# Optimization experiments

Hardware: AMD Instinct MI355X
Metric: run time of the kernel (lower is better)

The kernel has to match this reference:

```python
import jax, jax.numpy as jnp
import numpy as np

KNOTS = 16
BN_EPS = 1e-5  # flax BatchNorm default


def _normalize_spline_params(W, H, D):
    # widths/heights sum to 1 over the [0,1] hypercube; slopes positive
    dx = jax.nn.softmax(W, axis=-1)          # (N, d, K) bin widths
    dy = jax.nn.softmax(H, axis=-1)          # (N, d, K) bin heights
    sl = jax.nn.softplus(D)                  # (N, d, K-1) interior knot slopes
    return dx, dy, sl


def _gather_bin(a, idx):
    # a: (N, d, K'), idx: (N, d) -> (N, d)
    return jnp.take_along_axis(a, idx[..., None], axis=-1)[..., 0]


def _rqs_forward(t, dx, dy, sl):
    """Rational-quadratic spline on [0,1] (Durkan et al. 2019); identity outside.
    t: (N, d); dx, dy: (N, d, K); sl: (N, d, K-1).
    Returns y: (N, d), log_det: (N,)."""
    K = dx.shape[-1]
    zero = jnp.zeros_like(dx[..., :1])
    one = jnp.ones_like(dx[..., :1])
    xk = jnp.concatenate([zero, jnp.cumsum(dx, axis=-1)], axis=-1)   # (N, d, K+1) knot x
    yk = jnp.concatenate([zero, jnp.cumsum(dy, axis=-1)], axis=-1)   # (N, d, K+1) knot y
    dk = jnp.concatenate([one, sl, one], axis=-1)                    # (N, d, K+1) knot slopes

    in_bounds = (t >= 0.0) & (t <= 1.0)
    tc = jnp.clip(t, 0.0, 1.0)
    # per-element bin search (vectorized searchsorted)
    idx = jnp.clip(jnp.sum((tc[..., None] >= xk).astype(jnp.int32), axis=-1) - 1, 0, K - 1)

    xk_b = _gather_bin(xk, idx)
    yk_b = _gather_bin(yk, idx)
    dx_b = _gather_bin(dx, idx)
    dy_b = _gather_bin(dy, idx)
    d0 = _gather_bin(dk, idx)
    d1 = _gather_bin(dk, idx + 1)

    xi = (tc - xk_b) / dx_b            # position within bin, in [0,1]
    s = dy_b / dx_b                    # bin mean slope
    xi1m = xi * (1.0 - xi)
    den = s + (d0 + d1 - 2.0 * s) * xi1m
    y_in = yk_b + dy_b * (s * xi * xi + d0 * xi1m) / den
    dydx = s * s * (d1 * xi * xi + 2.0 * s * xi1m + d0 * (1.0 - xi) ** 2) / (den * den)

    y = jnp.where(in_bounds, y_in, t)
    log_det = jnp.sum(jnp.where(in_bounds, jnp.log(dydx), 0.0), axis=1)  # (N,)
    return y, log_det


def setup_inputs() -> dict:
    key = jax.random.key(0)
    ks = jax.random.split(key, 8)
    N, D, C = 65536, 64, 16
    d = D // 2
    spline_dim = 3 * KNOTS - 1
    cin = d + C           # conditioner input width: hstack(xc, c)
    H1, H2 = 128, 128     # layers=(128,128)

    def dense(k, fi, fo):
        return (jax.random.normal(k, (fi, fo), jnp.float32) / np.float32(np.sqrt(fi)))

    return {
        "x": jax.random.uniform(ks[0], (N, D), jnp.float32),
        "c": jax.random.normal(ks[1], (N, C), jnp.float32),
        "bn_scale": jnp.ones((cin,), jnp.float32),
        "bn_bias": jnp.zeros((cin,), jnp.float32),
        "bn_mean": 0.1 * jax.random.normal(ks[2], (cin,), jnp.float32),
        "bn_var": jax.random.uniform(ks[3], (cin,), jnp.float32, minval=0.5, maxval=1.5),
        "W0": dense(ks[4], cin, H1), "b0": jnp.zeros((H1,), jnp.float32),
        "W1": dense(ks[5], H1, H2), "b1": jnp.zeros((H2,), jnp.float32),
        "W2": dense(ks[6], H2, d * spline_dim), "b2": jnp.zeros((d * spline_dim,), jnp.float32),
    }


def reference(x, c, bn_scale, bn_bias, bn_mean, bn_var, W0, b0, W1, b1, W2, b2):
    N, D = x.shape
    d = D // 2
    xt, xc = x[:, :d], x[:, d:]
    h = jnp.hstack((xc, c))
    # BatchNorm in eval mode (use_running_average=True)
    h = (h - bn_mean) * jax.lax.rsqrt(bn_var + BN_EPS) * bn_scale + bn_bias
    h = jax.nn.swish(h @ W0 + b0)
    h = jax.nn.swish(h @ W1 + b1)
    p = (h @ W2 + b2).reshape(N, d, 3 * KNOTS - 1)
    dx, dy, sl = _normalize_spline_params(
        p[..., :KNOTS], p[..., KNOTS:2 * KNOTS], p[..., 2 * KNOTS:])
    yt, log_det = _rqs_forward(xt, dx, dy, sl)
    y = jnp.hstack((yt, xc))
    return y, log_det
```

## Files before the change

### kernel.cpp

```cpp
#include <hip/hip_runtime.h>
#include <math.h>

#define BN_EPS 1e-5f
#define ROWS 64

typedef __attribute__((ext_vector_type(8))) short short8;
typedef __attribute__((ext_vector_type(4))) float float4v;

__device__ __forceinline__ unsigned short f2bf(float f) {
    union { float f; unsigned int u; } v; v.f = f;
    unsigned int r = v.u + 0x7FFF + ((v.u >> 16) & 1);
    return (unsigned short)(r >> 16);
}
__device__ __forceinline__ float softplus_f(float v) {
    float r = log1pf(__expf(-fabsf(v)));
    return v > 0.f ? v + r : r;
}
__device__ __forceinline__ float swish_f(float a) {
    return a / (1.f + __expf(-a));
}

__global__ void prep_weights(const float* __restrict__ W0, const float* __restrict__ W1,
                             const float* __restrict__ W2,
                             unsigned short* __restrict__ Wt0, unsigned short* __restrict__ Wt1,
                             unsigned short* __restrict__ Wt2) {
    int e = blockIdx.x * 256 + threadIdx.x;
    if (e < 128 * 64) {
        int n = e >> 6, k = e & 63;
        Wt0[e] = f2bf(k < 48 ? W0[k * 128 + n] : 0.f);
        return;
    }
    e -= 128 * 64;
    if (e < 128 * 128) {
        int n = e >> 7, k = e & 127;
        Wt1[e] = f2bf(W1[k * 128 + n]);
        return;
    }
    e -= 128 * 128;
    if (e < 1536 * 128) {
        int col = e >> 7, k = e & 127;
        int d = col / 48, j = col - d * 48;
        Wt2[e] = f2bf(j < 47 ? W2[k * 1504 + d * 47 + j] : 0.f);
    }
}

__launch_bounds__(256, 2)
__global__ void nsc_mfma(const float* __restrict__ x, const float* __restrict__ c,
                         const float* __restrict__ bn_scale, const float* __restrict__ bn_bias,
                         const float* __restrict__ bn_mean, const float* __restrict__ bn_var,
                         const unsigned short* __restrict__ Wt0, const float* __restrict__ b0,
                         const unsigned short* __restrict__ Wt1, const float* __restrict__ b1,
                         const unsigned short* __restrict__ Wt2, const float* __restrict__ b2,
                         float* __restrict__ out, int N) {
    __shared__ char smem[70656];
    unsigned short* h0 = (unsigned short*)smem;
    unsigned short* h2 = (unsigned short*)smem;
    float*          yt = (float*)smem;
    float*          ldp = (float*)(smem + 8448);
    unsigned short* h1 = (unsigned short*)(smem + 17408);

    const int tid  = threadIdx.x;
    const int lane = tid & 63;
    const int l    = lane & 15;
    const int q    = lane >> 4;
    const int wu   = __builtin_amdgcn_readfirstlane(tid >> 6);
    const int r0   = blockIdx.x * ROWS;
    float* pw = (float*)(smem + 17408) + wu * (64 * 52);

    for (int idx = tid; idx < 64 * 64; idx += 256) {
        int r = idx >> 6, j = idx & 63;
        float h = 0.f;
        if (j < 48) {
            int row = r0 + r;
            float v = (j < 32) ? x[(size_t)row * 64 + 32 + j] : c[(size_t)row * 16 + (j - 32)];
            h = (v - bn_mean[j]) * rsqrtf(bn_var[j] + BN_EPS) * bn_scale[j] + bn_bias[j];
        }
        h0[r * 72 + j] = f2bf(h);
    }
    for (int idx = tid; idx < 64 * 32; idx += 256) {
        int r = idx >> 5, j = idx & 31;
        out[(size_t)(r0 + r) * 64 + 32 + j] = x[(size_t)(r0 + r) * 64 + 32 + j];
    }
    float xtreg[8];
    {
        const float* xrow = x + (size_t)(r0 + lane) * 64 + wu * 8;
        *(float4v*)(xtreg)     = *(const float4v*)(xrow);
        *(float4v*)(xtreg + 4) = *(const float4v*)(xrow + 4);
    }
    __syncthreads();

    {
        float4v acc[2][4];
        float4v z = {0.f, 0.f, 0.f, 0.f};
        #pragma unroll
        for (int nt = 0; nt < 2; ++nt)
            #pragma unroll
            for (int mt = 0; mt < 4; ++mt) acc[nt][mt] = z;
        #pragma unroll
        for (int ks = 0; ks < 2; ++ks) {
            short8 a[4];
            #pragma unroll
            for (int mt = 0; mt < 4; ++mt)
                a[mt] = *(const short8*)(h0 + (mt * 16 + l) * 72 + ks * 32 + (q << 3));
            #pragma unroll
            for (int nt = 0; nt < 2; ++nt) {
                int n0 = (wu * 2 + nt) * 16;
                short8 b = *(const short8*)(Wt0 + (n0 + l) * 64 + ks * 32 + (q << 3));
                #pragma unroll
                for (int mt = 0; mt < 4; ++mt)
                    acc[nt][mt] = __builtin_amdgcn_mfma_f32_16x16x32_bf16(a[mt], b, acc[nt][mt], 0, 0, 0);
            }
        }
        #pragma unroll
        for (int nt = 0; nt < 2; ++nt) {
            int n0 = (wu * 2 + nt) * 16;
            float bb = b0[n0 + l];
            #pragma unroll
            for (int mt = 0; mt < 4; ++mt)
                #pragma unroll
                for (int r = 0; r < 4; ++r)
                    h1[(mt * 16 + q * 4 + r) * 136 + n0 + l] = f2bf(swish_f(acc[nt][mt][r] + bb));
        }
    }
    __syncthreads();

    {
        float4v acc[2][4];
        float4v z = {0.f, 0.f, 0.f, 0.f};
        #pragma unroll
        for (int nt = 0; nt < 2; ++nt)
            #pragma unroll
            for (int mt = 0; mt < 4; ++mt) acc[nt][mt] = z;
        #pragma unroll
        for (int ks = 0; ks < 4; ++ks) {
            short8 a[4];
            #pragma unroll
            for (int mt = 0; mt < 4; ++mt)
                a[mt] = *(const short8*)(h1 + (mt * 16 + l) * 136 + ks * 32 + (q << 3));
            #pragma unroll
            for (int nt = 0; nt < 2; ++nt) {
                int n0 = (wu * 2 + nt) * 16;
                short8 b = *(const short8*)(Wt1 + (n0 + l) * 128 + ks * 32 + (q << 3));
                #pragma unroll
                for (int mt = 0; mt < 4; ++mt)
                    acc[nt][mt] = __builtin_amdgcn_mfma_f32_16x16x32_bf16(a[mt], b, acc[nt][mt], 0, 0, 0);
            }
        }
        #pragma unroll
        for (int nt = 0; nt < 2; ++nt) {
            int n0 = (wu * 2 + nt) * 16;
            float bb = b1[n0 + l];
            #pragma unroll
            for (int mt = 0; mt < 4; ++mt)
                #pragma unroll
                for (int r = 0; r < 4; ++r)
                    h2[(mt * 16 + q * 4 + r) * 136 + n0 + l] = f2bf(swish_f(acc[nt][mt][r] + bb));
        }
    }
    __syncthreads();

    short8 af[4][4];
    #pragma unroll
    for (int mt = 0; mt < 4; ++mt)
        #pragma unroll
        for (int ks = 0; ks < 4; ++ks)
            af[mt][ks] = *(const short8*)(h2 + (mt * 16 + l) * 136 + ks * 32 + (q << 3));
    __syncthreads();

    float ld_local = 0.f;
    for (int pass = 0; pass < 8; ++pass) {
        const int d  = wu * 8 + pass;
        const int cb = d * 48;
        float4v acc[3][4];
        float4v z = {0.f, 0.f, 0.f, 0.f};
        #pragma unroll
        for (int nt = 0; nt < 3; ++nt)
            #pragma unroll
            for (int mt = 0; mt < 4; ++mt) acc[nt][mt] = z;
        #pragma unroll
        for (int ks = 0; ks < 4; ++ks) {
            #pragma unroll
            for (int nt = 0; nt < 3; ++nt) {
                short8 b = *(const short8*)(Wt2 + (size_t)(cb + nt * 16 + l) * 128 + ks * 32 + (q << 3));
                #pragma unroll
                for (int mt = 0; mt < 4; ++mt)
                    acc[nt][mt] = __builtin_amdgcn_mfma_f32_16x16x32_bf16(af[mt][ks], b, acc[nt][mt], 0, 0, 0);
            }
        }
        #pragma unroll
        for (int nt = 0; nt < 3; ++nt) {
            int j = nt * 16 + l;
            float bj = (j < 47) ? b2[d * 47 + j] : 0.f;
            #pragma unroll
            for (int mt = 0; mt < 4; ++mt)
                #pragma unroll
                for (int r = 0; r < 4; ++r)
                    pw[(mt * 16 + q * 4 + r) * 52 + j] = acc[nt][mt][r] + bj;
        }
        asm volatile("s_waitcnt lgkmcnt(0)" ::: "memory");
        float pr[48];
        #pragma unroll
        for (int j = 0; j < 12; ++j)
            *(float4v*)(pr + j * 4) = *(const float4v*)(pw + lane * 52 + j * 4);

        float mWv = pr[0], mHv = pr[16];
        #pragma unroll
        for (int i = 1; i < 16; ++i) { mWv = fmaxf(mWv, pr[i]); mHv = fmaxf(mHv, pr[16 + i]); }
        float sW = 0.f, sH = 0.f;
        #pragma unroll
        for (int i = 0; i < 16; ++i) { pr[i] = __expf(pr[i] - mWv); sW += pr[i]; }
        #pragma unroll
        for (int i = 0; i < 16; ++i) { pr[16 + i] = __expf(pr[16 + i] - mHv); sH += pr[16 + i]; }
        float invW = 1.f / sW, invH = 1.f / sH;

        float t  = xtreg[pass];
        bool inb = (t >= 0.f) && (t <= 1.f);
        float tc = fminf(fmaxf(t, 0.f), 1.f);

        float cum = 0.f, cumy = 0.f, xkb = 0.f, ykb = 0.f;
        float dxb = pr[0] * invW, dyb = pr[16] * invH;
        int idx = 0;
        #pragma unroll
        for (int i = 0; i < 16; ++i) {
            float dxi = pr[i] * invW, dyi = pr[16 + i] * invH;
            bool cnd = (tc >= cum);
            idx = cnd ? i : idx;
            xkb = cnd ? cum : xkb;
            ykb = cnd ? cumy : ykb;
            dxb = cnd ? dxi : dxb;
            dyb = cnd ? dyi : dyb;
            cum  += dxi;
            cumy += dyi;
        }
        float a0 = 0.f, a1 = 0.f;
        #pragma unroll
        for (int j = 0; j < 15; ++j) {
            a0 = (j == idx - 1) ? pr[32 + j] : a0;
            a1 = (j == idx)     ? pr[32 + j] : a1;
        }
        float d0 = (idx == 0)  ? 1.f : softplus_f(a0);
        float d1 = (idx == 15) ? 1.f : softplus_f(a1);

        float xi  = (tc - xkb) / dxb;
        float s   = dyb / dxb;
        float xim = 1.f - xi;
        float x1m = xi * xim;
        float den = s + (d0 + d1 - 2.f * s) * x1m;
        float y_in = ykb + dyb * (s * xi * xi + d0 * x1m) / den;
        float dydx = s * s * (d1 * xi * xi + 2.f * s * x1m + d0 * xim * xim) / (den * den);

        yt[lane * 33 + d] = inb ? y_in : t;
        ld_local += inb ? __logf(dydx) : 0.f;
    }
    ldp[wu * 64 + lane] = ld_local;
    __syncthreads();

    for (int idx = tid; idx < 64 * 32; idx += 256) {
        int r = idx >> 5, j = idx & 31;
        out[(size_t)(r0 + r) * 64 + j] = yt[r * 33 + j];
    }
    if (tid < 64) {
        out[(size_t)N * 64 + r0 + tid] =
            ldp[tid] + ldp[64 + tid] + ldp[128 + tid] + ldp[192 + tid];
    }
}

extern "C" void kernel_launch(void* const* d_in, const int* in_sizes, int n_in,
                              void* d_out, int out_size, void* d_ws, size_t ws_size,
                              hipStream_t stream) {
    const float* x        = (const float*)d_in[0];
    const float* c        = (const float*)d_in[1];
    const float* bn_scale = (const float*)d_in[2];
    const float* bn_bias  = (const float*)d_in[3];
    const float* bn_mean  = (const float*)d_in[4];
    const float* bn_var   = (const float*)d_in[5];
    const float* W0       = (const float*)d_in[6];
    const float* b0       = (const float*)d_in[7];
    const float* W1       = (const float*)d_in[8];
    const float* b1       = (const float*)d_in[9];
    const float* W2       = (const float*)d_in[10];
    const float* b2       = (const float*)d_in[11];
    float* out = (float*)d_out;

    unsigned short* Wt0 = (unsigned short*)d_ws;
    unsigned short* Wt1 = Wt0 + 128 * 64;
    unsigned short* Wt2 = Wt1 + 128 * 128;

    const int N = in_sizes[0] / 64;
    prep_weights<<<(128 * 64 + 128 * 128 + 1536 * 128 + 255) / 256, 256, 0, stream>>>(
        W0, W1, W2, Wt0, Wt1, Wt2);
    nsc_mfma<<<N / ROWS, 256, 0, stream>>>(x, c, bn_scale, bn_bias, bn_mean, bn_var,
                                           Wt0, b0, Wt1, b1, Wt2, b2, out, N);
}
```

Before: 186.2 us.

## Cut LDS and registers to double occupancy in spline GEMM stage

Shrinks shared memory from about 70KB to 38KB and raises the launch bound from 2 to 4 blocks per CU. The final GEMM is transposed so each lane holds a row's outputs: the h2 fragments are reloaded from LDS on every pass instead of being kept in registers, and spline parameters are staged through a small 16-wide LDS tile one group at a time (widths, heights, slopes) rather than as all 48 values at once. Bias is pre-padded in the prep kernel for vector loads. y values are written straight from registers to global memory, and xt is loaded per pass. The aim is higher occupancy to hide latency, in exchange for more LDS reads per pass and tighter register pressure.

```diff
diff --git a/kernel.cpp b/kernel.cpp
--- a/kernel.cpp
+++ b/kernel.cpp
@@ -21,9 +21,9 @@
 }
 
 __global__ void prep_weights(const float* __restrict__ W0, const float* __restrict__ W1,
-                             const float* __restrict__ W2,
+                             const float* __restrict__ W2, const float* __restrict__ b2,
                              unsigned short* __restrict__ Wt0, unsigned short* __restrict__ Wt1,
-                             unsigned short* __restrict__ Wt2) {
+                             unsigned short* __restrict__ Wt2, float* __restrict__ b2p) {
     int e = blockIdx.x * 256 + threadIdx.x;
     if (e < 128 * 64) {
         int n = e >> 6, k = e & 63;
@@ -41,23 +41,28 @@
         int col = e >> 7, k = e & 127;
         int d = col / 48, j = col - d * 48;
         Wt2[e] = f2bf(j < 47 ? W2[k * 1504 + d * 47 + j] : 0.f);
-    }
-}
-
-__launch_bounds__(256, 2)
+        return;
+    }
+    e -= 1536 * 128;
+    if (e < 32 * 48) {
+        int d = e / 48, j = e - d * 48;
+        b2p[e] = (j < 47) ? b2[d * 47 + j] : 0.f;
+    }
+}
+
+__launch_bounds__(256, 4)
 __global__ void nsc_mfma(const float* __restrict__ x, const float* __restrict__ c,
                          const float* __restrict__ bn_scale, const float* __restrict__ bn_bias,
                          const float* __restrict__ bn_mean, const float* __restrict__ bn_var,
                          const unsigned short* __restrict__ Wt0, const float* __restrict__ b0,
                          const unsigned short* __restrict__ Wt1, const float* __restrict__ b1,
-                         const unsigned short* __restrict__ Wt2, const float* __restrict__ b2,
+                         const unsigned short* __restrict__ Wt2, const float* __restrict__ b2p,
                          float* __restrict__ out, int N) {
-    __shared__ char smem[70656];
+    __shared__ __align__(16) char smem[38912];
     unsigned short* h0 = (unsigned short*)smem;
     unsigned short* h2 = (unsigned short*)smem;
-    float*          yt = (float*)smem;
-    float*          ldp = (float*)(smem + 8448);
     unsigned short* h1 = (unsigned short*)(smem + 17408);
+    float*          ldp = (float*)(smem + 17408 + 20480);
 
     const int tid  = threadIdx.x;
     const int lane = tid & 63;
@@ -65,7 +70,7 @@
     const int q    = lane >> 4;
     const int wu   = __builtin_amdgcn_readfirstlane(tid >> 6);
     const int r0   = blockIdx.x * ROWS;
-    float* pw = (float*)(smem + 17408) + wu * (64 * 52);
+    float* pw = (float*)(smem + 17408) + wu * (64 * 20);
 
     for (int idx = tid; idx < 64 * 64; idx += 256) {
         int r = idx >> 6, j = idx & 63;
@@ -81,12 +86,6 @@
         int r = idx >> 5, j = idx & 31;
         out[(size_t)(r0 + r) * 64 + 32 + j] = x[(size_t)(r0 + r) * 64 + 32 + j];
     }
-    float xtreg[8];
-    {
-        const float* xrow = x + (size_t)(r0 + lane) * 64 + wu * 8;
-        *(float4v*)(xtreg)     = *(const float4v*)(xrow);
-        *(float4v*)(xtreg + 4) = *(const float4v*)(xrow + 4);
-    }
     __syncthreads();
 
     {
@@ -159,84 +158,105 @@
     }
     __syncthreads();
 
-    short8 af[4][4];
-    #pragma unroll
-    for (int mt = 0; mt < 4; ++mt)
-        #pragma unroll
-        for (int ks = 0; ks < 4; ++ks)
-            af[mt][ks] = *(const short8*)(h2 + (mt * 16 + l) * 136 + ks * 32 + (q << 3));
-    __syncthreads();
-
     float ld_local = 0.f;
+    float yreg[8];
     for (int pass = 0; pass < 8; ++pass) {
-        const int d  = wu * 8 + pass;
-        const int cb = d * 48;
+        const int d = wu * 8 + pass;
         float4v acc[3][4];
         float4v z = {0.f, 0.f, 0.f, 0.f};
         #pragma unroll
-        for (int nt = 0; nt < 3; ++nt)
-            #pragma unroll
-            for (int mt = 0; mt < 4; ++mt) acc[nt][mt] = z;
+        for (int jt = 0; jt < 3; ++jt)
+            #pragma unroll
+            for (int smt = 0; smt < 4; ++smt) acc[jt][smt] = z;
         #pragma unroll
         for (int ks = 0; ks < 4; ++ks) {
-            #pragma unroll
-            for (int nt = 0; nt < 3; ++nt) {
-                short8 b = *(const short8*)(Wt2 + (size_t)(cb + nt * 16 + l) * 128 + ks * 32 + (q << 3));
-                #pragma unroll
-                for (int mt = 0; mt < 4; ++mt)
-                    acc[nt][mt] = __builtin_amdgcn_mfma_f32_16x16x32_bf16(af[mt][ks], b, acc[nt][mt], 0, 0, 0);
+            short8 bf[4];
+            #pragma unroll
+            for (int smt = 0; smt < 4; ++smt)
+                bf[smt] = *(const short8*)(h2 + (smt * 16 + l) * 136 + ks * 32 + (q << 3));
+            #pragma unroll
+            for (int jt = 0; jt < 3; ++jt) {
+                short8 a = *(const short8*)(Wt2 + (size_t)(d * 48 + jt * 16 + l) * 128 + ks * 32 + (q << 3));
+                #pragma unroll
+                for (int smt = 0; smt < 4; ++smt)
+                    acc[jt][smt] = __builtin_amdgcn_mfma_f32_16x16x32_bf16(a, bf[smt], acc[jt][smt], 0, 0, 0);
             }
         }
-        #pragma unroll
-        for (int nt = 0; nt < 3; ++nt) {
-            int j = nt * 16 + l;
-            float bj = (j < 47) ? b2[d * 47 + j] : 0.f;
-            #pragma unroll
-            for (int mt = 0; mt < 4; ++mt)
-                #pragma unroll
-                for (int r = 0; r < 4; ++r)
-                    pw[(mt * 16 + q * 4 + r) * 52 + j] = acc[nt][mt][r] + bj;
-        }
-        asm volatile("s_waitcnt lgkmcnt(0)" ::: "memory");
-        float pr[48];
-        #pragma unroll
-        for (int j = 0; j < 12; ++j)
-            *(float4v*)(pr + j * 4) = *(const float4v*)(pw + lane * 52 + j * 4);
-
-        float mWv = pr[0], mHv = pr[16];
-        #pragma unroll
-        for (int i = 1; i < 16; ++i) { mWv = fmaxf(mWv, pr[i]); mHv = fmaxf(mHv, pr[16 + i]); }
-        float sW = 0.f, sH = 0.f;
-        #pragma unroll
-        for (int i = 0; i < 16; ++i) { pr[i] = __expf(pr[i] - mWv); sW += pr[i]; }
-        #pragma unroll
-        for (int i = 0; i < 16; ++i) { pr[16 + i] = __expf(pr[16 + i] - mHv); sH += pr[16 + i]; }
-        float invW = 1.f / sW, invH = 1.f / sH;
-
-        float t  = xtreg[pass];
+
+        float t  = x[(size_t)(r0 + lane) * 64 + d];
         bool inb = (t >= 0.f) && (t <= 1.f);
         float tc = fminf(fmaxf(t, 0.f), 1.f);
-
-        float cum = 0.f, cumy = 0.f, xkb = 0.f, ykb = 0.f;
-        float dxb = pr[0] * invW, dyb = pr[16] * invH;
+        float pr[16];
+
+        {
+            float4v bj = *(const float4v*)(b2p + d * 48 + (q << 2));
+            #pragma unroll
+            for (int smt = 0; smt < 4; ++smt)
+                *(float4v*)(pw + (smt * 16 + l) * 20 + (q << 2)) = acc[0][smt] + bj;
+            asm volatile("s_waitcnt lgkmcnt(0)" ::: "memory");
+            #pragma unroll
+            for (int c2 = 0; c2 < 4; ++c2)
+                *(float4v*)(pr + c2 * 4) = *(const float4v*)(pw + lane * 20 + c2 * 4);
+        }
+        float mW = pr[0];
+        #pragma unroll
+        for (int i = 1; i < 16; ++i) mW = fmaxf(mW, pr[i]);
+        float sW = 0.f;
+        #pragma unroll
+        for (int i = 0; i < 16; ++i) { pr[i] = __expf(pr[i] - mW); sW += pr[i]; }
+        float invW = 1.f / sW;
+        float cum = 0.f, xkb = 0.f, dxb = pr[0] * invW;
         int idx = 0;
         #pragma unroll
         for (int i = 0; i < 16; ++i) {
-            float dxi = pr[i] * invW, dyi = pr[16 + i] * invH;
+            float dxi = pr[i] * invW;
             bool cnd = (tc >= cum);
-            idx = cnd ? i : idx;
+            idx = cnd ? i   : idx;
             xkb = cnd ? cum : xkb;
-            ykb = cnd ? cumy : ykb;
             dxb = cnd ? dxi : dxb;
-            dyb = cnd ? dyi : dyb;
-            cum  += dxi;
-            cumy += dyi;
+            cum += dxi;
+        }
+
+        {
+            float4v bj = *(const float4v*)(b2p + d * 48 + 16 + (q << 2));
+            #pragma unroll
+            for (int smt = 0; smt < 4; ++smt)
+                *(float4v*)(pw + (smt * 16 + l) * 20 + (q << 2)) = acc[1][smt] + bj;
+            asm volatile("s_waitcnt lgkmcnt(0)" ::: "memory");
+            #pragma unroll
+            for (int c2 = 0; c2 < 4; ++c2)
+                *(float4v*)(pr + c2 * 4) = *(const float4v*)(pw + lane * 20 + c2 * 4);
+        }
+        float mH = pr[0];
+        #pragma unroll
+        for (int i = 1; i < 16; ++i) mH = fmaxf(mH, pr[i]);
+        float sH = 0.f;
+        #pragma unroll
+        for (int i = 0; i < 16; ++i) { pr[i] = __expf(pr[i] - mH); sH += pr[i]; }
+        float invH = 1.f / sH;
+        float ykb = 0.f, dyb = pr[0] * invH;
+        #pragma unroll
+        for (int i = 0; i < 16; ++i) {
+            float dyi = pr[i] * invH;
+            ykb += (i < idx) ? dyi : 0.f;
+            dyb  = (i == idx) ? dyi : dyb;
+        }
+
+        {
+            float4v bj = *(const float4v*)(b2p + d * 48 + 32 + (q << 2));
+            #pragma unroll
+            for (int smt = 0; smt < 4; ++smt)
+                *(float4v*)(pw + (smt * 16 + l) * 20 + (q << 2)) = acc[2][smt] + bj;
+            asm volatile("s_waitcnt lgkmcnt(0)" ::: "memory");
+            #pragma unroll
+            for (int c2 = 0; c2 < 4; ++c2)
+                *(float4v*)(pr + c2 * 4) = *(const float4v*)(pw + lane * 20 + c2 * 4);
         }
         float a0 = 0.f, a1 = 0.f;
         #pragma unroll
-        for (int j = 0; j < 15; ++j) {
-            a0 = (j == idx - 1) ? pr[32 + j] : a0;
-            a1 = (j == idx)     ? pr[32 + j] : a1;
+        for (int i = 0; i < 15; ++i) {
+            a0 = (i == idx - 1) ? pr[i] : a0;
+            a1 = (i == idx)     ? pr[i] : a1;
         }
         float d0 = (idx == 0)  ? 1.f : softplus_f(a0);
         float d1 = (idx == 15) ? 1.f : softplus_f(a1);
@@ -249,16 +269,17 @@
         float y_in = ykb + dyb * (s * xi * xi + d0 * x1m) / den;
         float dydx = s * s * (d1 * xi * xi + 2.f * s * x1m + d0 * xim * xim) / (den * den);
 
-        yt[lane * 33 + d] = inb ? y_in : t;
+        yreg[pass] = inb ? y_in : t;
         ld_local += inb ? __logf(dydx) : 0.f;
+    }
+
+    {
+        float4v* o = (float4v*)(out + (size_t)(r0 + lane) * 64 + wu * 8);
+        o[0] = *(const float4v*)(yreg);
+        o[1] = *(const float4v*)(yreg + 4);
     }
     ldp[wu * 64 + lane] = ld_local;
     __syncthreads();
-
-    for (int idx = tid; idx < 64 * 32; idx += 256) {
-        int r = idx >> 5, j = idx & 31;
-        out[(size_t)(r0 + r) * 64 + j] = yt[r * 33 + j];
-    }
     if (tid < 64) {
         out[(size_t)N * 64 + r0 + tid] =
             ldp[tid] + ldp[64 + tid] + ldp[128 + tid] + ldp[192 + tid];
@@ -285,10 +306,12 @@
     unsigned short* Wt0 = (unsigned short*)d_ws;
     unsigned short* Wt1 = Wt0 + 128 * 64;
     unsigned short* Wt2 = Wt1 + 128 * 128;
+    float*          b2p = (float*)(Wt2 + 1536 * 128);
 
     const int N = in_sizes[0] / 64;
-    prep_weights<<<(128 * 64 + 128 * 128 + 1536 * 128 + 255) / 256, 256, 0, stream>>>(
-        W0, W1, W2, Wt0, Wt1, Wt2);
+    const int prep_elems = 128 * 64 + 128 * 128 + 1536 * 128 + 32 * 48;
+    prep_weights<<<(prep_elems + 255) / 256, 256, 0, stream>>>(
+        W0, W1, W2, b2, Wt0, Wt1, Wt2, b2p);
     nsc_mfma<<<N / ROWS, 256, 0, stream>>>(x, c, bn_scale, bn_bias, bn_mean, bn_var,
-                                           Wt0, b0, Wt1, b1, Wt2, b2, out, N);
-}
+                                           Wt0, b0, Wt1, b1, Wt2, b2p, out, N);
+}
```

Result: faster. 172.0 us (-7.6%).
